# Kernel optimization log

Hardware: AMD Instinct MI355X
Metric: run time of the kernel (lower is better)

## Reference

```python
import jax, jax.numpy as jnp
import numpy as np

CLASSES = [20, 70, 250, 800, 3000, 12000]
DIM = 768
B = 2048


def setup_inputs() -> dict:
    key = jax.random.key(0)
    ks = jax.random.split(key, 2 * len(CLASSES) + 1)
    inp = {"x": jax.random.normal(ks[0], (B, DIM), jnp.float32)}
    scale = 1.0 / np.sqrt(DIM).astype(np.float32)
    for i, c in enumerate(CLASSES):
        # Concatenation of all per-node generator Linear layers at level i.
        inp[f"W{i}"] = jax.random.normal(ks[1 + i], (c, DIM), jnp.float32) * scale
        inp[f"b{i}"] = jnp.zeros((c,), jnp.float32)
    for lvl in range(1, 6):
        k = jax.random.fold_in(key, 100 + lvl)
        # parent index (at level lvl-1) of each class at level lvl; sorted -> contiguous sibling groups
        inp[f"p{lvl}"] = jnp.sort(
            jax.random.randint(k, (CLASSES[lvl],), 0, CLASSES[lvl - 1], jnp.int32)
        )
    return inp


def _segment_softmax_cols(logits, parent, num_parents):
    """Softmax over columns of logits [B, C], within groups of columns sharing a parent."""
    lt = logits.T  # [C, B]
    mx = jax.ops.segment_max(lt, parent, num_segments=num_parents)  # [P, B]
    e = jnp.exp(lt - mx[parent])
    s = jax.ops.segment_sum(e, parent, num_segments=num_parents)  # [P, B]
    return (e / s[parent]).T  # [B, C]


def reference(x, W0, b0, W1, b1, W2, b2, W3, b3, W4, b4, W5, b5, p1, p2, p3, p4, p5):
    # Level 0: root generator = Linear + Softmax over all level-0 classes.
    out = jax.nn.softmax(x @ W0.T + b0, axis=1)  # [B, classes[0]]
    outputs = [out]
    Ws = [W1, W2, W3, W4, W5]
    bs = [b1, b2, b3, b4, b5]
    ps = [p1, p2, p3, p4, p5]
    for lvl in range(5):
        logits = x @ Ws[lvl].T + bs[lvl]  # [B, classes[lvl+1]]
        cond = _segment_softmax_cols(logits, ps[lvl], CLASSES[lvl])  # per-parent softmax
        out = cond * outputs[-1][:, ps[lvl]]  # scatter of prob * subtree(x) == gather of parent prob
        outputs.append(out)
    return tuple(outputs)
```

## Files before the change

### kernel.cpp

```cpp
#include <hip/hip_runtime.h>
#include <stdint.h>

#define BDIM 2048
#define KDIM 768
#define NTOT 16140
#define NKT 24

typedef _Float16 half8 __attribute__((ext_vector_type(8)));
typedef float floatx4 __attribute__((ext_vector_type(4)));

__device__ __forceinline__ unsigned short f2h(float f) {
  _Float16 h = (_Float16)f;
  return __builtin_bit_cast(unsigned short, h);
}

__device__ __forceinline__ void level_of(int col, int& cb, int& Cl, long long& ob) {
  if      (col < 20)   { cb = 0;    Cl = 20;    ob = 0LL; }
  else if (col < 90)   { cb = 20;   Cl = 70;    ob = 40960LL; }
  else if (col < 340)  { cb = 90;   Cl = 250;   ob = 184320LL; }
  else if (col < 1140) { cb = 340;  Cl = 800;   ob = 696320LL; }
  else if (col < 4140) { cb = 1140; Cl = 3000;  ob = 2334720LL; }
  else                 { cb = 4140; Cl = 12000; ob = 8478720LL; }
}

__device__ __forceinline__ void gload_lds16(const void* g, void* l) {
  __builtin_amdgcn_global_load_lds(
      (const __attribute__((address_space(1))) unsigned int*)g,
      (__attribute__((address_space(3))) unsigned int*)l, 16, 0, 0);
}

__global__ __launch_bounds__(256) void convert_kernel(
    const float* __restrict__ x,
    const float* __restrict__ W0, const float* __restrict__ W1,
    const float* __restrict__ W2, const float* __restrict__ W3,
    const float* __restrict__ W4, const float* __restrict__ W5,
    unsigned short* __restrict__ xh, unsigned short* __restrict__ wh)
{
  long long i4 = (long long)blockIdx.x * 256 + threadIdx.x;
  if (i4 >= 3492096LL) return;
  long long e = i4 * 4;
  const long long XN = (long long)BDIM * KDIM;
  float4 v;
  unsigned short* dst;
  if (e < XN) {
    v = reinterpret_cast<const float4*>(x)[i4];
    dst = xh + e;
  } else {
    long long we = e - XN;
    const float* src; long long off;
    if      (we < 15360)    { src = W0; off = we; }
    else if (we < 69120)    { src = W1; off = we - 15360; }
    else if (we < 261120)   { src = W2; off = we - 69120; }
    else if (we < 875520)   { src = W3; off = we - 261120; }
    else if (we < 3179520)  { src = W4; off = we - 875520; }
    else                    { src = W5; off = we - 3179520; }
    v = reinterpret_cast<const float4*>(src)[off >> 2];
    dst = wh + we;
  }
  ushort4 o;
  o.x = f2h(v.x); o.y = f2h(v.y); o.z = f2h(v.z); o.w = f2h(v.w);
  *reinterpret_cast<ushort4*>(dst) = o;
}

__global__ __launch_bounds__(256) void seg_build_kernel(
    const int* __restrict__ p1, const int* __restrict__ p2, const int* __restrict__ p3,
    const int* __restrict__ p4, const int* __restrict__ p5, int* __restrict__ gst)
{
  int j = blockIdx.x * 256 + threadIdx.x;
  if (j > 4141) return;
  int val;
  if (j == 0) val = 0;
  else if (j == 4141) val = 16140;
  else {
    const int* p; int C, s, base;
    if      (j < 21)   { p = p1; C = 70;    s = j - 1;    base = 20; }
    else if (j < 91)   { p = p2; C = 250;   s = j - 21;   base = 90; }
    else if (j < 341)  { p = p3; C = 800;   s = j - 91;   base = 340; }
    else if (j < 1141) { p = p4; C = 3000;  s = j - 341;  base = 1140; }
    else               { p = p5; C = 12000; s = j - 1141; base = 4140; }
    int lo = 0, hi = C;
    while (lo < hi) { int mid = (lo + hi) >> 1; if (p[mid] < s) lo = mid + 1; else hi = mid; }
    val = base + lo;
  }
  gst[j] = val;
}

#define EPI_STRIDE 132

__global__ __launch_bounds__(256, 2) void gemm_kernel(
    const unsigned short* __restrict__ Ah,
    const unsigned short* __restrict__ Wh,
    float* __restrict__ out)
{
  __shared__ __align__(16) char smem_raw[64 * EPI_STRIDE * 4];
  float* epi = (float*)smem_raw;

  const int bid = blockIdx.x;
  const int logical = (bid & 7) * 254 + (bid >> 3);
  const int cx = logical >> 4;
  const int row0 = (logical & 15) * 128;
  const int col0 = cx * 128;

  const int tid  = threadIdx.x;
  const int wave = tid >> 6;
  const int lane = tid & 63;
  const int wr = (wave >> 1) * 64;
  const int wc = (wave & 1) * 64;
  const int q  = lane >> 4;
  const int lr = lane & 15;

  const int rquad = lane >> 2;
  const int kq = lane & 3;

  floatx4 acc[4][4];
#pragma unroll
  for (int i = 0; i < 4; ++i)
#pragma unroll
    for (int j = 0; j < 4; ++j)
      acc[i][j] = (floatx4){0.f, 0.f, 0.f, 0.f};

  const unsigned short* gA[2];
  const unsigned short* gB[2];
#pragma unroll
  for (int i = 0; i < 2; ++i) {
    int c = 2 * wave + i;
    int rowA = row0 + 16 * c + rquad;
    gA[i] = Ah + (long long)rowA * KDIM + kq * 8;
    int colB = col0 + 16 * c + rquad;
    if (colB >= NTOT) colB = NTOT - 1;
    gB[i] = Wh + (long long)colB * KDIM + kq * 8;
  }

  auto stage = [&](int buf, int kt) {
#pragma unroll
    for (int i = 0; i < 2; ++i) {
      int c = 2 * wave + i;
      gload_lds16(gA[i] + kt * 32, smem_raw + buf * 8192 + c * 1024);
      gload_lds16(gB[i] + kt * 32, smem_raw + 16384 + buf * 8192 + c * 1024);
    }
  };

  int cur = 0;
  stage(0, 0);
  __syncthreads();

  for (int kt = 0; kt < NKT; ++kt) {
    if (kt + 1 < NKT) stage(cur ^ 1, kt + 1);
    const char* Ac = smem_raw + cur * 8192;
    const char* Bc = smem_raw + 16384 + cur * 8192;
    half8 af[4], bf[4];
#pragma unroll
    for (int i = 0; i < 4; ++i)
      af[i] = __builtin_bit_cast(half8, *(const uint4*)(Ac + (wr + i * 16 + lr) * 64 + q * 16));
#pragma unroll
    for (int j = 0; j < 4; ++j)
      bf[j] = __builtin_bit_cast(half8, *(const uint4*)(Bc + (wc + j * 16 + lr) * 64 + q * 16));
#pragma unroll
    for (int i = 0; i < 4; ++i)
#pragma unroll
      for (int j = 0; j < 4; ++j)
        acc[i][j] = __builtin_amdgcn_mfma_f32_16x16x32_f16(af[i], bf[j], acc[i][j], 0, 0, 0);
    __syncthreads();
    cur ^= 1;
  }

  int cbA, ClA; long long obA; level_of(col0, cbA, ClA, obA);
  int cbB, ClB; long long obB; level_of(col0 + 127, cbB, ClB, obB);
  const bool fast = (cbA == cbB) && ((cbA & 3) == 0) && ((ClA & 3) == 0) && (col0 + 128 <= NTOT);

  for (int h = 0; h < 2; ++h) {
    __syncthreads();
    if ((wave >> 1) == h) {
#pragma unroll
      for (int i = 0; i < 4; ++i)
#pragma unroll
        for (int j = 0; j < 4; ++j)
#pragma unroll
          for (int rg = 0; rg < 4; ++rg)
            epi[(i * 16 + q * 4 + rg) * EPI_STRIDE + wc + j * 16 + lr] = acc[i][j][rg];
    }
    __syncthreads();
    if (fast) {
      const long long rowbase = obA + (long long)(row0 + h * 64) * ClA + (col0 - cbA);
#pragma unroll
      for (int it = 0; it < 8; ++it) {
        int idx = it * 256 + tid;
        int r = idx >> 5, f4 = idx & 31;
        float4 v = *(const float4*)(epi + r * EPI_STRIDE + f4 * 4);
        *(float4*)(out + rowbase + (long long)r * ClA + f4 * 4) = v;
      }
    } else {
      for (int idx = tid; idx < 64 * 128; idx += 256) {
        int r = idx >> 7, c = idx & 127;
        int col = col0 + c;
        if (col < NTOT) {
          int cb, Cl; long long ob; level_of(col, cb, Cl, ob);
          out[ob + (long long)(row0 + h * 64 + r) * Cl + (col - cb)] = epi[r * EPI_STRIDE + c];
        }
      }
    }
  }
}

__global__ __launch_bounds__(512) void tree_softmax_kernel(
    float* __restrict__ out,
    const float* __restrict__ b0, const float* __restrict__ b1, const float* __restrict__ b2,
    const float* __restrict__ b3, const float* __restrict__ b4, const float* __restrict__ b5,
    const int* __restrict__ gst,
    const int* __restrict__ p1, const int* __restrict__ p2, const int* __restrict__ p3,
    const int* __restrict__ p4, const int* __restrict__ p5)
{
  __shared__ __align__(16) float l[NTOT];
  __shared__ __align__(16) float S[4141];
  const int tid = threadIdx.x;
  const long long row = blockIdx.x;

  if (tid < 340) {
    float v;
    if      (tid < 20) v = out[row * 20 + tid] + b0[tid];
    else if (tid < 90) v = out[40960 + row * 70 + (tid - 20)] + b1[tid - 20];
    else               v = out[184320 + row * 250 + (tid - 90)] + b2[tid - 90];
    l[tid] = __expf(v);
  }
  if (tid < 200) {
    float4 v = reinterpret_cast<const float4*>(out + 696320 + row * 800)[tid];
    float4 b = reinterpret_cast<const float4*>(b3)[tid];
    float4 e;
    e.x = __expf(v.x + b.x); e.y = __expf(v.y + b.y);
    e.z = __expf(v.z + b.z); e.w = __expf(v.w + b.w);
    reinterpret_cast<float4*>(l + 340)[tid] = e;
  }
  for (int i4 = tid; i4 < 750; i4 += 512) {
    float4 v = reinterpret_cast<const float4*>(out + 2334720 + row * 3000)[i4];
    float4 b = reinterpret_cast<const float4*>(b4)[i4];
    float4 e;
    e.x = __expf(v.x + b.x); e.y = __expf(v.y + b.y);
    e.z = __expf(v.z + b.z); e.w = __expf(v.w + b.w);
    reinterpret_cast<float4*>(l + 1140)[i4] = e;
  }
  for (int i4 = tid; i4 < 3000; i4 += 512) {
    float4 v = reinterpret_cast<const float4*>(out + 8478720 + row * 12000)[i4];
    float4 b = reinterpret_cast<const float4*>(b5)[i4];
    float4 e;
    e.x = __expf(v.x + b.x); e.y = __expf(v.y + b.y);
    e.z = __expf(v.z + b.z); e.w = __expf(v.w + b.w);
    reinterpret_cast<float4*>(l + 4140)[i4] = e;
  }
  __syncthreads();

  for (int j = tid; j < 4141; j += 512) {
    int a = gst[j], b = gst[j + 1];
    float s = 0.f;
    for (int c = a; c < b; ++c) s += l[c];
    S[j] = s;
  }
  __syncthreads();

  if (tid < 20) {
    float s0 = S[0];
    float inv = 1.f / s0;
    float t = l[tid] * inv / S[1 + tid];
    S[1 + tid] = t;
    if (tid == 0) S[0] = inv;
  }
  __syncthreads();
  if (tid < 70)
    S[21 + tid] = l[20 + tid] * S[1 + p1[tid]] / S[21 + tid];
  __syncthreads();
  if (tid < 250)
    S[91 + tid] = l[90 + tid] * S[21 + p2[tid]] / S[91 + tid];
  __syncthreads();
  for (int s = tid; s < 800; s += 512)
    S[341 + s] = l[340 + s] * S[91 + p3[s]] / S[341 + s];
  __syncthreads();
  for (int s = tid; s < 3000; s += 512)
    S[1141 + s] = l[1140 + s] * S[341 + p4[s]] / S[1141 + s];
  __syncthreads();

  if (tid < 340) {
    if (tid < 20)      out[row * 20 + tid] = l[tid] * S[0];
    else if (tid < 90) out[40960 + row * 70 + (tid - 20)] = l[tid] * S[1 + p1[tid - 20]];
    else               out[184320 + row * 250 + (tid - 90)] = l[tid] * S[21 + p2[tid - 90]];
  }
  if (tid < 200) {
    int4 p = reinterpret_cast<const int4*>(p3)[tid];
    float4 e = reinterpret_cast<const float4*>(l + 340)[tid];
    e.x *= S[91 + p.x]; e.y *= S[91 + p.y]; e.z *= S[91 + p.z]; e.w *= S[91 + p.w];
    reinterpret_cast<float4*>(out + 696320 + row * 800)[tid] = e;
  }
  for (int i4 = tid; i4 < 750; i4 += 512) {
    int4 p = reinterpret_cast<const int4*>(p4)[i4];
    float4 e = reinterpret_cast<const float4*>(l + 1140)[i4];
    e.x *= S[341 + p.x]; e.y *= S[341 + p.y]; e.z *= S[341 + p.z]; e.w *= S[341 + p.w];
    reinterpret_cast<float4*>(out + 2334720 + row * 3000)[i4] = e;
  }
  for (int i4 = tid; i4 < 3000; i4 += 512) {
    int4 p = reinterpret_cast<const int4*>(p5)[i4];
    float4 e = reinterpret_cast<const float4*>(l + 4140)[i4];
    e.x *= S[1141 + p.x]; e.y *= S[1141 + p.y]; e.z *= S[1141 + p.z]; e.w *= S[1141 + p.w];
    reinterpret_cast<float4*>(out + 8478720 + row * 12000)[i4] = e;
  }
}

extern "C" void kernel_launch(void* const* d_in, const int* in_sizes, int n_in,
                              void* d_out, int out_size, void* d_ws, size_t ws_size,
                              hipStream_t stream)
{
  const float* x = (const float*)d_in[0];
  const float* W[6]    = {(const float*)d_in[1], (const float*)d_in[3], (const float*)d_in[5],
                          (const float*)d_in[7], (const float*)d_in[9], (const float*)d_in[11]};
  const float* bias[6] = {(const float*)d_in[2], (const float*)d_in[4], (const float*)d_in[6],
                          (const float*)d_in[8], (const float*)d_in[10], (const float*)d_in[12]};
  const int* p[5] = {(const int*)d_in[13], (const int*)d_in[14], (const int*)d_in[15],
                     (const int*)d_in[16], (const int*)d_in[17]};
  float* out = (float*)d_out;
  char* ws = (char*)d_ws;
  unsigned short* xh = (unsigned short*)ws;
  unsigned short* wh = (unsigned short*)(ws + 3145728);
  int* gst = (int*)(ws + 27936768);

  seg_build_kernel<<<17, 256, 0, stream>>>(p[0], p[1], p[2], p[3], p[4], gst);
  convert_kernel<<<13641, 256, 0, stream>>>(x, W[0], W[1], W[2], W[3], W[4], W[5], xh, wh);
  gemm_kernel<<<2032, 256, 0, stream>>>(xh, wh, out);
  tree_softmax_kernel<<<2048, 512, 0, stream>>>(
      out, bias[0], bias[1], bias[2], bias[3], bias[4], bias[5], gst,
      p[0], p[1], p[2], p[3], p[4]);
}
```

Baseline: 358.7 us.

## Drop per-row LDS logits buffer, recompute exps from global; merge prep kernels

The tree softmax kernel no longer stages all 16140 exponentiated logits per row in shared memory. Instead it recomputes exp(logit+bias) from global memory in the segment-sum pass, the per-level probability pass and the final write pass. This cuts LDS use from about 81KB to about 16KB per block so more blocks fit per CU, at the cost of reading each row's logits twice and doing extra exp work with strided per-segment global loads. The segment-boundary build is also merged with the fp16 conversion into one prep kernel, which additionally builds a concatenated bias array, removing one launch.

```diff
diff --git a/kernel.cpp b/kernel.cpp
--- a/kernel.cpp
+++ b/kernel.cpp
@@ -29,60 +29,77 @@
       (__attribute__((address_space(3))) unsigned int*)l, 16, 0, 0);
 }
 
-__global__ __launch_bounds__(256) void convert_kernel(
+__global__ __launch_bounds__(256) void prep_kernel(
     const float* __restrict__ x,
     const float* __restrict__ W0, const float* __restrict__ W1,
     const float* __restrict__ W2, const float* __restrict__ W3,
     const float* __restrict__ W4, const float* __restrict__ W5,
-    unsigned short* __restrict__ xh, unsigned short* __restrict__ wh)
+    const float* __restrict__ b0, const float* __restrict__ b1, const float* __restrict__ b2,
+    const float* __restrict__ b3, const float* __restrict__ b4, const float* __restrict__ b5,
+    const int* __restrict__ p1, const int* __restrict__ p2, const int* __restrict__ p3,
+    const int* __restrict__ p4, const int* __restrict__ p5,
+    unsigned short* __restrict__ xh, unsigned short* __restrict__ wh,
+    int* __restrict__ gst, float* __restrict__ bcat)
 {
   long long i4 = (long long)blockIdx.x * 256 + threadIdx.x;
-  if (i4 >= 3492096LL) return;
-  long long e = i4 * 4;
-  const long long XN = (long long)BDIM * KDIM;
-  float4 v;
-  unsigned short* dst;
-  if (e < XN) {
-    v = reinterpret_cast<const float4*>(x)[i4];
-    dst = xh + e;
-  } else {
-    long long we = e - XN;
-    const float* src; long long off;
-    if      (we < 15360)    { src = W0; off = we; }
-    else if (we < 69120)    { src = W1; off = we - 15360; }
-    else if (we < 261120)   { src = W2; off = we - 69120; }
-    else if (we < 875520)   { src = W3; off = we - 261120; }
-    else if (we < 3179520)  { src = W4; off = we - 875520; }
-    else                    { src = W5; off = we - 3179520; }
-    v = reinterpret_cast<const float4*>(src)[off >> 2];
-    dst = wh + we;
-  }
-  ushort4 o;
-  o.x = f2h(v.x); o.y = f2h(v.y); o.z = f2h(v.z); o.w = f2h(v.w);
-  *reinterpret_cast<ushort4*>(dst) = o;
-}
-
-__global__ __launch_bounds__(256) void seg_build_kernel(
-    const int* __restrict__ p1, const int* __restrict__ p2, const int* __restrict__ p3,
-    const int* __restrict__ p4, const int* __restrict__ p5, int* __restrict__ gst)
-{
-  int j = blockIdx.x * 256 + threadIdx.x;
-  if (j > 4141) return;
-  int val;
-  if (j == 0) val = 0;
-  else if (j == 4141) val = 16140;
-  else {
-    const int* p; int C, s, base;
-    if      (j < 21)   { p = p1; C = 70;    s = j - 1;    base = 20; }
-    else if (j < 91)   { p = p2; C = 250;   s = j - 21;   base = 90; }
-    else if (j < 341)  { p = p3; C = 800;   s = j - 91;   base = 340; }
-    else if (j < 1141) { p = p4; C = 3000;  s = j - 341;  base = 1140; }
-    else               { p = p5; C = 12000; s = j - 1141; base = 4140; }
-    int lo = 0, hi = C;
-    while (lo < hi) { int mid = (lo + hi) >> 1; if (p[mid] < s) lo = mid + 1; else hi = mid; }
-    val = base + lo;
-  }
-  gst[j] = val;
+  if (i4 < 3492096LL) {
+    long long e = i4 * 4;
+    const long long XN = (long long)BDIM * KDIM;
+    float4 v;
+    unsigned short* dst;
+    if (e < XN) {
+      v = reinterpret_cast<const float4*>(x)[i4];
+      dst = xh + e;
+    } else {
+      long long we = e - XN;
+      const float* src; long long off;
+      if      (we < 15360)    { src = W0; off = we; }
+      else if (we < 69120)    { src = W1; off = we - 15360; }
+      else if (we < 261120)   { src = W2; off = we - 69120; }
+      else if (we < 875520)   { src = W3; off = we - 261120; }
+      else if (we < 3179520)  { src = W4; off = we - 875520; }
+      else                    { src = W5; off = we - 3179520; }
+      v = reinterpret_cast<const float4*>(src)[off >> 2];
+      dst = wh + we;
+    }
+    ushort4 o;
+    o.x = f2h(v.x); o.y = f2h(v.y); o.z = f2h(v.z); o.w = f2h(v.w);
+    *reinterpret_cast<ushort4*>(dst) = o;
+    return;
+  }
+  long long u = i4 - 3492096LL;
+  if (u < 4142) {
+    int j = (int)u;
+    int val;
+    if (j == 0) val = 0;
+    else if (j == 4141) val = 16140;
+    else {
+      const int* p; int C, s, base;
+      if      (j < 21)   { p = p1; C = 70;    s = j - 1;    base = 20; }
+      else if (j < 91)   { p = p2; C = 250;   s = j - 21;   base = 90; }
+      else if (j < 341)  { p = p3; C = 800;   s = j - 91;   base = 340; }
+      else if (j < 1141) { p = p4; C = 3000;  s = j - 341;  base = 1140; }
+      else               { p = p5; C = 12000; s = j - 1141; base = 4140; }
+      int lo = 0, hi = C;
+      while (lo < hi) { int mid = (lo + hi) >> 1; if (p[mid] < s) lo = mid + 1; else hi = mid; }
+      val = base + lo;
+    }
+    gst[j] = val;
+    return;
+  }
+  long long v5 = u - 4142;
+  if (v5 < 16140) {
+    int col = (int)v5;
+    int cb, Cl; long long ob; level_of(col, cb, Cl, ob);
+    const float* bs;
+    if      (col < 20)   bs = b0;
+    else if (col < 90)   bs = b1;
+    else if (col < 340)  bs = b2;
+    else if (col < 1140) bs = b3;
+    else if (col < 4140) bs = b4;
+    else                 bs = b5;
+    bcat[col] = bs[col - cb];
+  }
 }
 
 #define EPI_STRIDE 132
@@ -204,100 +221,95 @@
 
 __global__ __launch_bounds__(512) void tree_softmax_kernel(
     float* __restrict__ out,
-    const float* __restrict__ b0, const float* __restrict__ b1, const float* __restrict__ b2,
-    const float* __restrict__ b3, const float* __restrict__ b4, const float* __restrict__ b5,
-    const int* __restrict__ gst,
+    const float* __restrict__ bcat, const int* __restrict__ gst,
     const int* __restrict__ p1, const int* __restrict__ p2, const int* __restrict__ p3,
     const int* __restrict__ p4, const int* __restrict__ p5)
 {
-  __shared__ __align__(16) float l[NTOT];
-  __shared__ __align__(16) float S[4141];
+  __shared__ float S[4141];
   const int tid = threadIdx.x;
   const long long row = blockIdx.x;
 
+  for (int j = tid; j < 4141; j += 512) {
+    int a = gst[j], b = gst[j + 1];
+    long long base; int cb, C;
+    if      (j == 0)   { base = 0LL;       cb = 0;    C = 20; }
+    else if (j < 21)   { base = 40960LL;   cb = 20;   C = 70; }
+    else if (j < 91)   { base = 184320LL;  cb = 90;   C = 250; }
+    else if (j < 341)  { base = 696320LL;  cb = 340;  C = 800; }
+    else if (j < 1141) { base = 2334720LL; cb = 1140; C = 3000; }
+    else               { base = 8478720LL; cb = 4140; C = 12000; }
+    const float* gb = out + base + row * C - cb;
+    float s = 0.f;
+    for (int c = a; c < b; ++c) s += __expf(gb[c] + bcat[c]);
+    S[j] = s;
+  }
+  __syncthreads();
+
+  if (tid < 20) {
+    float inv = 1.f / S[0];
+    float e0 = __expf(out[row * 20 + tid] + bcat[tid]);
+    S[1 + tid] = e0 * inv / S[1 + tid];
+    if (tid == 0) S[0] = inv;
+  }
+  __syncthreads();
+  if (tid < 70) {
+    float e1 = __expf(out[40960 + row * 70 + tid] + bcat[20 + tid]);
+    S[21 + tid] = e1 * S[1 + p1[tid]] / S[21 + tid];
+  }
+  __syncthreads();
+  if (tid < 250) {
+    float e2 = __expf(out[184320 + row * 250 + tid] + bcat[90 + tid]);
+    S[91 + tid] = e2 * S[21 + p2[tid]] / S[91 + tid];
+  }
+  __syncthreads();
+  for (int s = tid; s < 800; s += 512) {
+    float e3 = __expf(out[696320 + row * 800 + s] + bcat[340 + s]);
+    S[341 + s] = e3 * S[91 + p3[s]] / S[341 + s];
+  }
+  __syncthreads();
+  for (int s = tid; s < 3000; s += 512) {
+    float e4 = __expf(out[2334720 + row * 3000 + s] + bcat[1140 + s]);
+    S[1141 + s] = e4 * S[341 + p4[s]] / S[1141 + s];
+  }
+  __syncthreads();
+
   if (tid < 340) {
-    float v;
-    if      (tid < 20) v = out[row * 20 + tid] + b0[tid];
-    else if (tid < 90) v = out[40960 + row * 70 + (tid - 20)] + b1[tid - 20];
-    else               v = out[184320 + row * 250 + (tid - 90)] + b2[tid - 90];
-    l[tid] = __expf(v);
+    float p;
+    if (tid < 20)
+      p = __expf(out[row * 20 + tid] + bcat[tid]) * S[0];
+    else if (tid < 90)
+      p = __expf(out[40960 + row * 70 + (tid - 20)] + bcat[tid]) * S[1 + p1[tid - 20]];
+    else
+      p = __expf(out[184320 + row * 250 + (tid - 90)] + bcat[tid]) * S[21 + p2[tid - 90]];
+    if (tid < 20)      out[row * 20 + tid] = p;
+    else if (tid < 90) out[40960 + row * 70 + (tid - 20)] = p;
+    else               out[184320 + row * 250 + (tid - 90)] = p;
   }
   if (tid < 200) {
     float4 v = reinterpret_cast<const float4*>(out + 696320 + row * 800)[tid];
-    float4 b = reinterpret_cast<const float4*>(b3)[tid];
+    float4 b = reinterpret_cast<const float4*>(bcat + 340)[tid];
+    int4  p = reinterpret_cast<const int4*>(p3)[tid];
     float4 e;
-    e.x = __expf(v.x + b.x); e.y = __expf(v.y + b.y);
-    e.z = __expf(v.z + b.z); e.w = __expf(v.w + b.w);
-    reinterpret_cast<float4*>(l + 340)[tid] = e;
+    e.x = __expf(v.x + b.x) * S[91 + p.x]; e.y = __expf(v.y + b.y) * S[91 + p.y];
+    e.z = __expf(v.z + b.z) * S[91 + p.z]; e.w = __expf(v.w + b.w) * S[91 + p.w];
+    reinterpret_cast<float4*>(out + 696320 + row * 800)[tid] = e;
   }
   for (int i4 = tid; i4 < 750; i4 += 512) {
     float4 v = reinterpret_cast<const float4*>(out + 2334720 + row * 3000)[i4];
-    float4 b = reinterpret_cast<const float4*>(b4)[i4];
+    float4 b = reinterpret_cast<const float4*>(bcat + 1140)[i4];
+    int4  p = reinterpret_cast<const int4*>(p4)[i4];
     float4 e;
-    e.x = __expf(v.x + b.x); e.y = __expf(v.y + b.y);
-    e.z = __expf(v.z + b.z); e.w = __expf(v.w + b.w);
-    reinterpret_cast<float4*>(l + 1140)[i4] = e;
+    e.x = __expf(v.x + b.x) * S[341 + p.x]; e.y = __expf(v.y + b.y) * S[341 + p.y];
+    e.z = __expf(v.z + b.z) * S[341 + p.z]; e.w = __expf(v.w + b.w) * S[341 + p.w];
+    reinterpret_cast<float4*>(out + 2334720 + row * 3000)[i4] = e;
   }
   for (int i4 = tid; i4 < 3000; i4 += 512) {
     float4 v = reinterpret_cast<const float4*>(out + 8478720 + row * 12000)[i4];
-    float4 b = reinterpret_cast<const float4*>(b5)[i4];
+    float4 b = reinterpret_cast<const float4*>(bcat + 4140)[i4];
+    int4  p = reinterpret_cast<const int4*>(p5)[i4];
     float4 e;
-    e.x = __expf(v.x + b.x); e.y = __expf(v.y + b.y);
-    e.z = __expf(v.z + b.z); e.w = __expf(v.w + b.w);
-    reinterpret_cast<float4*>(l + 4140)[i4] = e;
-  }
-  __syncthreads();
-
-  for (int j = tid; j < 4141; j += 512) {
-    int a = gst[j], b = gst[j + 1];
-    float s = 0.f;
-    for (int c = a; c < b; ++c) s += l[c];
-    S[j] = s;
-  }
-  __syncthreads();
-
-  if (tid < 20) {
-    float s0 = S[0];
-    float inv = 1.f / s0;
-    float t = l[tid] * inv / S[1 + tid];
-    S[1 + tid] = t;
-    if (tid == 0) S[0] = inv;
-  }
-  __syncthreads();
-  if (tid < 70)
-    S[21 + tid] = l[20 + tid] * S[1 + p1[tid]] / S[21 + tid];
-  __syncthreads();
-  if (tid < 250)
-    S[91 + tid] = l[90 + tid] * S[21 + p2[tid]] / S[91 + tid];
-  __syncthreads();
-  for (int s = tid; s < 800; s += 512)
-    S[341 + s] = l[340 + s] * S[91 + p3[s]] / S[341 + s];
-  __syncthreads();
-  for (int s = tid; s < 3000; s += 512)
-    S[1141 + s] = l[1140 + s] * S[341 + p4[s]] / S[1141 + s];
-  __syncthreads();
-
-  if (tid < 340) {
-    if (tid < 20)      out[row * 20 + tid] = l[tid] * S[0];
-    else if (tid < 90) out[40960 + row * 70 + (tid - 20)] = l[tid] * S[1 + p1[tid - 20]];
-    else               out[184320 + row * 250 + (tid - 90)] = l[tid] * S[21 + p2[tid - 90]];
-  }
-  if (tid < 200) {
-    int4 p = reinterpret_cast<const int4*>(p3)[tid];
-    float4 e = reinterpret_cast<const float4*>(l + 340)[tid];
-    e.x *= S[91 + p.x]; e.y *= S[91 + p.y]; e.z *= S[91 + p.z]; e.w *= S[91 + p.w];
-    reinterpret_cast<float4*>(out + 696320 + row * 800)[tid] = e;
-  }
-  for (int i4 = tid; i4 < 750; i4 += 512) {
-    int4 p = reinterpret_cast<const int4*>(p4)[i4];
-    float4 e = reinterpret_cast<const float4*>(l + 1140)[i4];
-    e.x *= S[341 + p.x]; e.y *= S[341 + p.y]; e.z *= S[341 + p.z]; e.w *= S[341 + p.w];
-    reinterpret_cast<float4*>(out + 2334720 + row * 3000)[i4] = e;
-  }
-  for (int i4 = tid; i4 < 3000; i4 += 512) {
-    int4 p = reinterpret_cast<const int4*>(p5)[i4];
-    float4 e = reinterpret_cast<const float4*>(l + 4140)[i4];
-    e.x *= S[1141 + p.x]; e.y *= S[1141 + p.y]; e.z *= S[1141 + p.z]; e.w *= S[1141 + p.w];
+    e.x = __expf(v.x + b.x) * S[1141 + p.x]; e.y = __expf(v.y + b.y) * S[1141 + p.y];
+    e.z = __expf(v.z + b.z) * S[1141 + p.z]; e.w = __expf(v.w + b.w) * S[1141 + p.w];
     reinterpret_cast<float4*>(out + 8478720 + row * 12000)[i4] = e;
   }
 }
@@ -318,11 +330,13 @@
   unsigned short* xh = (unsigned short*)ws;
   unsigned short* wh = (unsigned short*)(ws + 3145728);
   int* gst = (int*)(ws + 27936768);
-
-  seg_build_kernel<<<17, 256, 0, stream>>>(p[0], p[1], p[2], p[3], p[4], gst);
-  convert_kernel<<<13641, 256, 0, stream>>>(x, W[0], W[1], W[2], W[3], W[4], W[5], xh, wh);
+  float* bcat = (float*)(ws + 27953344);
+
+  prep_kernel<<<13721, 256, 0, stream>>>(
+      x, W[0], W[1], W[2], W[3], W[4], W[5],
+      bias[0], bias[1], bias[2], bias[3], bias[4], bias[5],
+      p[0], p[1], p[2], p[3], p[4], xh, wh, gst, bcat);
   gemm_kernel<<<2032, 256, 0, stream>>>(xh, wh, out);
   tree_softmax_kernel<<<2048, 512, 0, stream>>>(
-      out, bias[0], bias[1], bias[2], bias[3], bias[4], bias[5], gst,
-      p[0], p[1], p[2], p[3], p[4]);
-}
+      out, bcat, gst, p[0], p[1], p[2], p[3], p[4]);
+}
```

New measurement: 376.7 us. +5.0%, slower.
